# Optimization experiments

Hardware: AMD Instinct MI355X
Metric: run time of the kernel (lower is better)

The kernel has to match this reference:

```python
import jax, jax.numpy as jnp
import numpy as np

NEG = -1e9  # effective -inf in log space (finite to keep grads NaN-free)


def _forward_lattice(theta, A):
    """alpha[b,i,j,s]: log-prob of all alignments reaching cell (i,j) in state s.
    States: 0=match (diag move), 1=insert-x (down move), 2=insert-y (right move).
    alpha[i,j,s] = theta[i,j,s] + LSE_k(alpha[i-ds,j-dj,k] + A[k,s]).
    Start: only the match contribution at (0,0) gets log-prob 0."""
    B, N, M, S = theta.shape
    j_is0 = (jnp.arange(M) == 0)  # [M]

    def row_step(prev_row, xs):
        theta_row, i = xs  # theta_row: [B, M, S]
        # diag predecessor alpha[i-1, j-1, :]
        diag = jnp.concatenate(
            [jnp.full((B, 1, S), NEG, theta_row.dtype), prev_row[:, :-1]], axis=1)
        lse_m = jax.nn.logsumexp(diag + A[:, None, :, 0], axis=-1)      # [B, M]
        lse_m = jnp.where((i == 0) & j_is0[None, :], 0.0, lse_m)        # start at (0,0)
        lse_x = jax.nn.logsumexp(prev_row + A[:, None, :, 1], axis=-1)  # [B, M]
        m_vals = theta_row[:, :, 0] + lse_m
        x_vals = theta_row[:, :, 1] + lse_x
        th_y = theta_row[:, :, 2]

        def col_step(left, cxs):
            # left: alpha[i, j-1, :] -> [B, S]
            m_j, x_j, ty_j = cxs  # each [B]
            y_j = ty_j + jax.nn.logsumexp(left + A[:, :, 2], axis=-1)
            cell = jnp.stack([m_j, x_j, y_j], axis=-1)  # [B, S]
            return cell, cell

        left0 = jnp.full((B, S), NEG, theta_row.dtype)
        _, row = jax.lax.scan(col_step, left0, (m_vals.T, x_vals.T, th_y.T))
        row = jnp.transpose(row, (1, 0, 2))  # [B, M, S]
        return row, row

    prev0 = jnp.full((B, M, S), NEG, theta.dtype)
    _, alpha = jax.lax.scan(row_step, prev0, (jnp.swapaxes(theta, 0, 1), jnp.arange(N)))
    return jnp.swapaxes(alpha, 0, 1)  # [B, N, M, S]


def _backward_lattice(theta, A):
    """beta[b,i,j,s]: log-prob of all alignment suffixes from (i,j) in state s.
    beta[i,j,s] = LSE( A[s,0]+theta[i+1,j+1,0]+beta[i+1,j+1,0],
                       A[s,1]+theta[i+1,j,1]  +beta[i+1,j,1],
                       A[s,2]+theta[i,j+1,2]  +beta[i,j+1,2] ),  beta[N-1,M-1,:] = 0.
    Computed as a forward scan on the flipped grid with u = beta + theta."""
    B, N, M, S = theta.shape
    theta_f = theta[:, ::-1, ::-1]
    j_is0 = (jnp.arange(M) == 0)

    def row_step(u_prev, xs):
        th_row, p = xs  # th_row: [B, M, S] (flipped coords)
        t_m = jnp.concatenate(
            [jnp.full((B, 1), NEG, th_row.dtype), u_prev[:, :-1, 0]], axis=1)  # [B, M]
        t_x = u_prev[:, :, 1]  # [B, M]

        def col_step(left_u2, cxs):
            tm_j, tx_j, th_j, j0 = cxs  # [B], [B], [B,S], scalar bool
            v = jnp.stack([tm_j, tx_j, left_u2], axis=-1)     # [B, S] over successor k
            g = jax.nn.logsumexp(A + v[:, None, :], axis=-1)  # [B, S]
            g = jnp.where((p == 0) & j0, 0.0, g)              # terminal cell
            u = g + th_j
            return u[:, 2], (g, u)

        left0 = jnp.full((B,), NEG, th_row.dtype)
        _, (g_row, u_row) = jax.lax.scan(
            col_step, left0, (t_m.T, t_x.T, jnp.swapaxes(th_row, 0, 1), j_is0))
        return jnp.transpose(u_row, (1, 0, 2)), jnp.transpose(g_row, (1, 0, 2))

    u0 = jnp.full((B, M, S), NEG, theta.dtype)
    _, g = jax.lax.scan(row_step, u0, (jnp.swapaxes(theta_f, 0, 1), jnp.arange(N)))
    g = jnp.swapaxes(g, 0, 1)  # [B, N, M, S] flipped coords
    return g[:, ::-1, ::-1]


def setup_inputs() -> dict:
    key = jax.random.key(0)
    k1, k2 = jax.random.split(key)
    B, N, M, S = 256, 128, 128, 3
    theta = jax.random.normal(k1, (B, N, M, S), dtype=jnp.float32)
    A = jax.random.normal(k2, (B, S, S), dtype=jnp.float32)
    return {"theta": theta, "A": A}


def reference(theta, A):
    # Baum-Welch: posterior log-marginals gamma = alpha + beta - logZ
    alpha = _forward_lattice(theta, A)
    beta = _backward_lattice(theta, A)
    logZ = jax.nn.logsumexp(alpha[:, -1, -1, :], axis=-1)  # [B]
    return alpha + beta - logZ[:, None, None, None]
```

## Files before the change

kernel.cpp:

```cpp
#include <hip/hip_runtime.h>

#define HNEG (-1000000000.0f)
#define HNEG2 (-1.44269504e9f)
#define INVLN2 1.44269504088896341f
#define LN2F 0.69314718055994531f

constexpr int Nc = 128;
constexpr int Mc = 128;
constexpr int CELLS = Nc * Mc * 3;
constexpr int AWSTRIDE = CELLS + 16;

__device__ __forceinline__ float ex2(float x) {
  return __builtin_amdgcn_exp2f(x);
}
__device__ __forceinline__ float lg2(float x) {
  return __builtin_amdgcn_logf(x);
}

__device__ __forceinline__ float lse3(float a, float b, float c) {
  float mx = fmaxf(fmaxf(a, b), c);
  return mx + __logf(__expf(a - mx) + __expf(b - mx) + __expf(c - mx));
}

__device__ __forceinline__ float shr1f(float src, float fill) {
  return __int_as_float(__builtin_amdgcn_update_dpp(
      __float_as_int(fill), __float_as_int(src), 0x138, 0xF, 0xF, false));
}

__device__ __forceinline__ int clamp127(int i) {
  return i < 0 ? 0 : (i > 127 ? 127 : i);
}

__device__ __forceinline__ void st3_even(float* o, float a, float b, float c) {
  *(float2*)o = make_float2(a, b);
  o[2] = c;
}
__device__ __forceinline__ void st3_odd(float* o, float a, float b, float c) {
  o[0] = a;
  *(float2*)(o + 1) = make_float2(b, c);
}

#define DECL6(p) float p##0, p##1, p##2, p##3, p##4, p##5


#define F2LOAD(P, dd) do {                                                     \
    const int dc_ = (dd) > 254 ? 254 : (dd);                                   \
    const int ca_ = clamp127(dc_ - jA), cb_ = clamp127(dc_ - jB);              \
    const float* pa_ = th + (ca_ * Mc + jA) * 3;                               \
    const float* pb_ = th + (cb_ * Mc + jB) * 3;                               \
    P##0 = pa_[0]; P##1 = pa_[1]; P##2 = pa_[2];                               \
    P##3 = pb_[0]; P##4 = pb_[1]; P##5 = pb_[2];                               \
  } while (0)

#define F2STEP(P, dd) do {                                                     \
    const int iA_ = (dd) - jA, iB_ = (dd) - jB;                                \
    const bool okA_ = (unsigned)iA_ < (unsigned)Nc;                            \
    const bool okB_ = (unsigned)iB_ < (unsigned)Nc;                            \
    const float g0 = mS2 + lg2(wS20 * E00 + wS21 * E10 + wS22 * E20);          \
    const float g1 = mPA + lg2(wPA0 * E01 + wPA1 * E11 + wPA2 * E21);          \
    const float g2 = mS1 + lg2(wS10 * E02 + wS11 * E12 + wS12 * E22);          \
    const float cA0 = okA_ ? fmaf(P##0, INVLN2, g0) : HNEG2;                   \
    const float cA1 = okA_ ? fmaf(P##1, INVLN2, g1) : HNEG2;                   \
    const float cA2 = okA_ ? fmaf(P##2, INVLN2, g2) : HNEG2;                   \
    st3_even(okA_ ? aw + (iA_ * Mc + jA) * 3 : dmpE, cA0, cA1, cA2);           \
    const float h0 = mPP + lg2(wPP0 * E00 + wPP1 * E10 + wPP2 * E20);          \
    const float h1 = mPB + lg2(wPB0 * E01 + wPB1 * E11 + wPB2 * E21);          \
    const float h2 = mPA + lg2(wPA0 * E02 + wPA1 * E12 + wPA2 * E22);          \
    const float cB0 = okB_ ? fmaf(P##3, INVLN2, h0) : HNEG2;                   \
    const float cB1 = okB_ ? fmaf(P##4, INVLN2, h1) : HNEG2;                   \
    const float cB2 = okB_ ? fmaf(P##5, INVLN2, h2) : HNEG2;                   \
    st3_odd(okB_ ? aw + (iB_ * Mc + jB) * 3 : dmpO, cB0, cB1, cB2);            \
    const float mA_ = fmaxf(fmaxf(cA0, cA1), cA2);                             \
    const float a0_ = ex2(cA0 - mA_), a1_ = ex2(cA1 - mA_),                    \
                a2_ = ex2(cA2 - mA_);                                          \
    const float mB_ = fmaxf(fmaxf(cB0, cB1), cB2);                             \
    const float b0_ = ex2(cB0 - mB_), b1_ = ex2(cB1 - mB_),                    \
                b2_ = ex2(cB2 - mB_);                                          \
    mPP = mPA; wPP0 = wPA0; wPP1 = wPA1; wPP2 = wPA2;                          \
    mPA = mA_; wPA0 = a0_; wPA1 = a1_; wPA2 = a2_;                             \
    mPB = mB_; wPB0 = b0_; wPB1 = b1_; wPB2 = b2_;                             \
    mS2 = mS1; wS20 = wS10; wS21 = wS11; wS22 = wS12;                          \
    mS1 = shr1f(mB_, HNEG2);                                                   \
    wS10 = shr1f(b0_, 1.f); wS11 = shr1f(b1_, 1.f); wS12 = shr1f(b2_, 1.f);    \
  } while (0)

#define B2LOADL(Pt, dd) do {                                                   \
    int dor_ = 254 - (dd); if (dor_ < 0) dor_ = 0;                             \
    const int ca_ = clamp127(dor_ - jjA), cb_ = clamp127(dor_ - jjB);          \
    const float* pa_ = th + (ca_ * Mc + jjA) * 3;                              \
    const float* pb_ = th + (cb_ * Mc + jjB) * 3;                              \
    Pt##0 = pa_[0]; Pt##1 = pa_[1]; Pt##2 = pa_[2];                            \
    Pt##3 = pb_[0]; Pt##4 = pb_[1]; Pt##5 = pb_[2];                            \
  } while (0)

#define B2STEPL(Pt, dd) do {                                                   \
    const int iA_ = Nc - 1 - (dd) + jA;                                        \
    const int iB_ = Nc - 1 - (dd) + jB;                                        \
    const bool okA_ = (unsigned)iA_ < (unsigned)Nc;                            \
    const bool okB_ = (unsigned)iB_ < (unsigned)Nc;                            \
    float uA0, uA1, uA2, uB0, uB1, uB2;                                        \
    {                                                                          \
      const float v0 = S2u0, v1 = pAu1, v2 = S1u2;                             \
      const float mv = fmaxf(fmaxf(v0, v1), v2);                               \
      const float w0 = ex2(v0 - mv), w1 = ex2(v1 - mv), w2 = ex2(v2 - mv);     \
      float g0 = mv + lg2(w0 * E00 + w1 * E01 + w2 * E02);                     \
      float g1 = mv + lg2(w0 * E10 + w1 * E11 + w2 * E12);                     \
      float g2 = mv + lg2(w0 * E20 + w1 * E21 + w2 * E22);                     \
      if ((dd) == 0 && l == 0) { g0 = 0.f; g1 = 0.f; g2 = 0.f; }               \
      uA0 = okA_ ? fmaf(Pt##0, INVLN2, g0) : HNEG2;                            \
      uA1 = okA_ ? fmaf(Pt##1, INVLN2, g1) : HNEG2;                            \
      uA2 = okA_ ? fmaf(Pt##2, INVLN2, g2) : HNEG2;                            \
      st3_odd(okA_ ? ob + (iA_ * Mc + jjA) * 3 : dmpO, g0, g1, g2);            \
    }                                                                          \
    {                                                                          \
      const float v0 = ppAu0, v1 = pBu1, v2 = pAu2;                            \
      const float mv = fmaxf(fmaxf(v0, v1), v2);                               \
      const float w0 = ex2(v0 - mv), w1 = ex2(v1 - mv), w2 = ex2(v2 - mv);     \
      const float g0 = mv + lg2(w0 * E00 + w1 * E01 + w2 * E02);               \
      const float g1 = mv + lg2(w0 * E10 + w1 * E11 + w2 * E12);               \
      const float g2 = mv + lg2(w0 * E20 + w1 * E21 + w2 * E22);               \
      uB0 = okB_ ? fmaf(Pt##3, INVLN2, g0) : HNEG2;                            \
      uB1 = okB_ ? fmaf(Pt##4, INVLN2, g1) : HNEG2;                            \
      uB2 = okB_ ? fmaf(Pt##5, INVLN2, g2) : HNEG2;                            \
      st3_even(okB_ ? ob + (iB_ * Mc + jjB) * 3 : dmpE, g0, g1, g2);           \
    }                                                                          \
    ppAu0 = pAu0; pAu0 = uA0; pAu1 = uA1; pAu2 = uA2; pBu1 = uB1;              \
    S2u0 = S1u0;                                                               \
    S1u0 = shr1f(uB0, HNEG2);                                                  \
    S1u2 = shr1f(uB2, HNEG2);                                                  \
  } while (0)

__global__ __launch_bounds__(128, 1) void fbf_kernel(
    const float* __restrict__ theta, const float* __restrict__ A,
    float* __restrict__ aw_, float* __restrict__ ob_) {
  const int b = blockIdx.x;
  const int wave = threadIdx.x >> 6;
  const int l = threadIdx.x & 63;
  const float* th = theta + (size_t)b * CELLS;
  const float* Ab = A + b * 9;
  const float E00 = __expf(Ab[0]), E01 = __expf(Ab[1]), E02 = __expf(Ab[2]);
  const float E10 = __expf(Ab[3]), E11 = __expf(Ab[4]), E12 = __expf(Ab[5]);
  const float E20 = __expf(Ab[6]), E21 = __expf(Ab[7]), E22 = __expf(Ab[8]);

  __shared__ float sLZ;

  const int jA = 2 * l, jB = 2 * l + 1;
  float* aw = aw_ + (size_t)b * AWSTRIDE;
  float* ob = ob_ + (size_t)b * CELLS;
  float* dpad = aw + CELLS;

  if (wave == 0) {
    float* dmpE = dpad;
    float* dmpO = dpad + 3;

    float mPA = HNEG2, wPA0 = 1.f, wPA1 = 1.f, wPA2 = 1.f;
    float mPB = HNEG2, wPB0 = 1.f, wPB1 = 1.f, wPB2 = 1.f;
    float mPP = HNEG2, wPP0 = 1.f, wPP1 = 1.f, wPP2 = 1.f;
    float mS1 = HNEG2, wS10 = 1.f, wS11 = 1.f, wS12 = 1.f;
    float mS2 = HNEG2, wS20 = 1.f, wS21 = 1.f, wS22 = 1.f;
    if (l == 0) { mS2 = 0.f; wS20 = 1.0f / E00; wS21 = 0.f; wS22 = 0.f; }

    DECL6(xt0); DECL6(xt1); DECL6(xt2); DECL6(xt3);
    DECL6(yt0); DECL6(yt1); DECL6(yt2); DECL6(yt3);

    F2LOAD(xt0, 0); F2LOAD(xt1, 1); F2LOAD(xt2, 2); F2LOAD(xt3, 3);
    F2LOAD(yt0, 4); F2LOAD(yt1, 5); F2LOAD(yt2, 6); F2LOAD(yt3, 7);

    for (int t = 0; t < 31; ++t) {
      const int d0 = 8 * t;
      F2STEP(xt0, d0 + 0); F2STEP(xt1, d0 + 1); F2STEP(xt2, d0 + 2); F2STEP(xt3, d0 + 3);
      F2LOAD(xt0, d0 + 8); F2LOAD(xt1, d0 + 9); F2LOAD(xt2, d0 + 10); F2LOAD(xt3, d0 + 11);
      F2STEP(yt0, d0 + 4); F2STEP(yt1, d0 + 5); F2STEP(yt2, d0 + 6); F2STEP(yt3, d0 + 7);
      F2LOAD(yt0, d0 + 12); F2LOAD(yt1, d0 + 13); F2LOAD(yt2, d0 + 14); F2LOAD(yt3, d0 + 15);
    }
    F2STEP(xt0, 248); F2STEP(xt1, 249); F2STEP(xt2, 250); F2STEP(xt3, 251);
    F2STEP(yt0, 252); F2STEP(yt1, 253); F2STEP(yt2, 254);
    if (l == 63) sLZ = mPB + lg2(wPB0 + wPB1 + wPB2);
  } else {
    const int jjA = Mc - 1 - jA, jjB = Mc - 1 - jB;
    float* dmpE = dpad + 8;
    float* dmpO = dpad + 11;

    float pAu0 = HNEG2, pAu1 = HNEG2, pAu2 = HNEG2;
    float ppAu0 = HNEG2, pBu1 = HNEG2;
    float S1u0 = HNEG2, S1u2 = HNEG2, S2u0 = HNEG2;

    DECL6(xt0); DECL6(xt1); DECL6(xt2); DECL6(xt3);
    DECL6(yt0); DECL6(yt1); DECL6(yt2); DECL6(yt3);

    B2LOADL(xt0, 0); B2LOADL(xt1, 1); B2LOADL(xt2, 2); B2LOADL(xt3, 3);
    B2LOADL(yt0, 4); B2LOADL(yt1, 5); B2LOADL(yt2, 6); B2LOADL(yt3, 7);

    for (int t = 0; t < 31; ++t) {
      const int d0 = 8 * t;
      B2STEPL(xt0, d0 + 0); B2STEPL(xt1, d0 + 1);
      B2STEPL(xt2, d0 + 2); B2STEPL(xt3, d0 + 3);
      B2LOADL(xt0, d0 + 8); B2LOADL(xt1, d0 + 9);
      B2LOADL(xt2, d0 + 10); B2LOADL(xt3, d0 + 11);
      B2STEPL(yt0, d0 + 4); B2STEPL(yt1, d0 + 5);
      B2STEPL(yt2, d0 + 6); B2STEPL(yt3, d0 + 7);
      B2LOADL(yt0, d0 + 12); B2LOADL(yt1, d0 + 13);
      B2LOADL(yt2, d0 + 14); B2LOADL(yt3, d0 + 15);
    }
    B2STEPL(xt0, 248); B2STEPL(xt1, 249); B2STEPL(xt2, 250); B2STEPL(xt3, 251);
    B2STEPL(yt0, 252); B2STEPL(yt1, 253); B2STEPL(yt2, 254);
  }

  __syncthreads();
  const float lz = sLZ;
  const float4* a4 = (const float4*)aw;
  float4* o4 = (float4*)ob;
#pragma unroll 4
  for (int k = threadIdx.x; k < CELLS / 4; k += 128) {
    const float4 a = a4[k];
    const float4 g = o4[k];
    o4[k] = make_float4((a.x + g.x - lz) * LN2F, (a.y + g.y - lz) * LN2F,
                        (a.z + g.z - lz) * LN2F, (a.w + g.w - lz) * LN2F);
  }
}

__global__ __launch_bounds__(128) void fwd_fb(const float* __restrict__ theta,
                                              const float* __restrict__ A,
                                              float* __restrict__ out) {
  const int b = blockIdx.x;
  const int j = threadIdx.x;
  const float* th = theta + (size_t)b * CELLS;
  float* ob = out + (size_t)b * CELLS;

  __shared__ float sA[9];
  __shared__ float ring[3][Mc + 1][3];
  if (j < 9) sA[j] = A[b * 9 + j];
  {
    float* rf = &ring[0][0][0];
    for (int t = j; t < 3 * (Mc + 1) * 3; t += Mc) rf[t] = HNEG;
  }
  __syncthreads();
  const float A00 = sA[0], A01 = sA[1], A02 = sA[2];
  const float A10 = sA[3], A11 = sA[4], A12 = sA[5];
  const float A20 = sA[6], A21 = sA[7], A22 = sA[8];

  float p0 = HNEG, p1 = HNEG, p2 = HNEG;
  float tc0 = 0.f, tc1 = 0.f, tc2 = 0.f, tn0 = 0.f, tn1 = 0.f, tn2 = 0.f;
  if (j == 0) { tc0 = th[0]; tc1 = th[1]; tc2 = th[2]; }
  if (j <= 1) {
    const int i1 = 1 - j;
    const float* p = th + (i1 * Mc + j) * 3;
    tn0 = p[0]; tn1 = p[1]; tn2 = p[2];
  }
  int s0 = 0, s1 = 2, s2 = 1;
  for (int d = 0; d < Nc + Mc - 1; ++d) {
    const int i = d - j;
    float tf0 = 0.f, tf1 = 0.f, tf2 = 0.f;
    const int ip = i + 2;
    if (ip >= 0 && ip < Nc) {
      const float* p = th + (ip * Mc + j) * 3;
      tf0 = p[0]; tf1 = p[1]; tf2 = p[2];
    }
    float c0 = HNEG, c1 = HNEG, c2 = HNEG;
    if (i >= 0 && i < Nc) {
      const float* nd1 = ring[s1][j];
      const float* nd2 = ring[s2][j];
      float lm = lse3(nd2[0] + A00, nd2[1] + A10, nd2[2] + A20);
      if (i == 0 && j == 0) lm = 0.0f;
      float lx = lse3(p0 + A01, p1 + A11, p2 + A21);
      float ly = lse3(nd1[0] + A02, nd1[1] + A12, nd1[2] + A22);
      c0 = tc0 + lm; c1 = tc1 + lx; c2 = tc2 + ly;
      float* o = ob + (i * Mc + j) * 3;
      o[0] = c0; o[1] = c1; o[2] = c2;
    }
    float* w = ring[s0][j + 1];
    w[0] = c0; w[1] = c1; w[2] = c2;
    __syncthreads();
    p0 = c0; p1 = c1; p2 = c2;
    tc0 = tn0; tc1 = tn1; tc2 = tn2;
    tn0 = tf0; tn1 = tf1; tn2 = tf2;
    const int t = s2; s2 = s1; s1 = s0; s0 = t;
  }
}

__global__ __launch_bounds__(128) void bwd_fb(const float* __restrict__ theta,
                                              const float* __restrict__ A,
                                              float* __restrict__ ob_) {
  const int b = blockIdx.x;
  const int q = threadIdx.x;
  const float* th = theta + (size_t)b * CELLS;
  float* ob = ob_ + (size_t)b * CELLS;

  __shared__ float sA[9];
  __shared__ float ring[3][Mc + 1][3];
  __shared__ float sZ;
  if (q < 9) sA[q] = A[b * 9 + q];
  {
    float* rf = &ring[0][0][0];
    for (int t = q; t < 3 * (Mc + 1) * 3; t += Mc) rf[t] = HNEG;
  }
  if (q == 0) {
    sZ = lse3(ob[(Nc * Mc - 1) * 3 + 0], ob[(Nc * Mc - 1) * 3 + 1],
              ob[(Nc * Mc - 1) * 3 + 2]);
  }
  __syncthreads();
  const float A00 = sA[0], A01 = sA[1], A02 = sA[2];
  const float A10 = sA[3], A11 = sA[4], A12 = sA[5];
  const float A20 = sA[6], A21 = sA[7], A22 = sA[8];
  const float logZ = sZ;

  const int jj = Mc - 1 - q;
  float pu1 = HNEG;
  float tc0 = 0.f, tc1 = 0.f, tc2 = 0.f, tn0 = 0.f, tn1 = 0.f, tn2 = 0.f;
  float ac0 = 0.f, ac1 = 0.f, ac2 = 0.f, an0 = 0.f, an1 = 0.f, an2 = 0.f;
  if (q == 0) {
    const float* p = th + ((Nc - 1) * Mc + jj) * 3;
    tc0 = p[0]; tc1 = p[1]; tc2 = p[2];
    const float* a = ob + ((Nc - 1) * Mc + jj) * 3;
    ac0 = a[0]; ac1 = a[1]; ac2 = a[2];
  }
  if (q <= 1) {
    const int i1 = Nc - 2 + q;
    const float* p = th + (i1 * Mc + jj) * 3;
    tn0 = p[0]; tn1 = p[1]; tn2 = p[2];
    const float* a = ob + (i1 * Mc + jj) * 3;
    an0 = a[0]; an1 = a[1]; an2 = a[2];
  }
  int s0 = 0, s1 = 2, s2 = 1;
  for (int d = 0; d < Nc + Mc - 1; ++d) {
    const int p = d - q;
    const int i = Nc - 1 - p;
    float tf0 = 0.f, tf1 = 0.f, tf2 = 0.f, af0 = 0.f, af1 = 0.f, af2 = 0.f;
    const int ipf = i - 2;
    if (ipf >= 0 && ipf < Nc) {
      const float* pp = th + (ipf * Mc + jj) * 3;
      tf0 = pp[0]; tf1 = pp[1]; tf2 = pp[2];
      const float* aa = ob + (ipf * Mc + jj) * 3;
      af0 = aa[0]; af1 = aa[1]; af2 = aa[2];
    }
    float u0 = HNEG, u1 = HNEG, u2 = HNEG;
    if (p >= 0 && p < Nc) {
      const float* nd1 = ring[s1][q];
      const float* nd2 = ring[s2][q];
      const float v0 = nd2[0];
      const float v1 = pu1;
      const float v2 = nd1[2];
      float g0 = lse3(A00 + v0, A01 + v1, A02 + v2);
      float g1 = lse3(A10 + v0, A11 + v1, A12 + v2);
      float g2 = lse3(A20 + v0, A21 + v1, A22 + v2);
      if (p == 0 && q == 0) { g0 = 0.0f; g1 = 0.0f; g2 = 0.0f; }
      u0 = g0 + tc0; u1 = g1 + tc1; u2 = g2 + tc2;
      float* o = ob + (i * Mc + jj) * 3;
      o[0] = ac0 + g0 - logZ;
      o[1] = ac1 + g1 - logZ;
      o[2] = ac2 + g2 - logZ;
    }
    float* w = ring[s0][q + 1];
    w[0] = u0; w[1] = u1; w[2] = u2;
    __syncthreads();
    pu1 = u1;
    tc0 = tn0; tc1 = tn1; tc2 = tn2;
    tn0 = tf0; tn1 = tf1; tn2 = tf2;
    ac0 = an0; ac1 = an1; ac2 = an2;
    an0 = af0; an1 = af1; an2 = af2;
    const int t = s2; s2 = s1; s1 = s0; s0 = t;
  }
}

extern "C" void kernel_launch(void* const* d_in, const int* in_sizes, int n_in,
                              void* d_out, int out_size, void* d_ws, size_t ws_size,
                              hipStream_t stream) {
  const float* theta = (const float*)d_in[0];
  const float* A = (const float*)d_in[1];
  float* out = (float*)d_out;
  const int B = in_sizes[1] / 9;

  const size_t need = (size_t)B * AWSTRIDE * 4;
  if (ws_size >= need) {
    float* aw = (float*)d_ws;
    fbf_kernel<<<dim3(B), dim3(128), 0, stream>>>(theta, A, aw, out);
  } else {
    fwd_fb<<<dim3(B), dim3(128), 0, stream>>>(theta, A, out);
    bwd_fb<<<dim3(B), dim3(128), 0, stream>>>(theta, A, out);
  }
}
```

Before: 203.4 us.

## Split final alpha+beta combine into a separate wide-grid kernel

The fused kernel no longer runs the final elementwise combine with only 128 threads per batch after the DP. Instead it writes logZ to workspace, and a second kernel with a grid of B x 12 blocks of 256 threads does the combine. The aim is to spread this bandwidth-bound pass across many more waves and CUs instead of two waves per block. The cost is an extra kernel launch and one more pass of reads through global memory between kernels.

Result: slower. 211.9 us (+4.2%).

```diff
diff --git a/kernel.cpp b/kernel.cpp
--- a/kernel.cpp
+++ b/kernel.cpp
@@ -130,9 +130,10 @@
     S1u2 = shr1f(uB2, HNEG2);                                                  \
   } while (0)
 
-__global__ __launch_bounds__(128, 1) void fbf_kernel(
+__global__ __launch_bounds__(128, 1) void fb_dp_kernel(
     const float* __restrict__ theta, const float* __restrict__ A,
-    float* __restrict__ aw_, float* __restrict__ ob_) {
+    float* __restrict__ aw_, float* __restrict__ logZ_ws,
+    float* __restrict__ ob_) {
   const int b = blockIdx.x;
   const int wave = threadIdx.x >> 6;
   const int l = threadIdx.x & 63;
@@ -142,8 +143,6 @@
   const float E10 = __expf(Ab[3]), E11 = __expf(Ab[4]), E12 = __expf(Ab[5]);
   const float E20 = __expf(Ab[6]), E21 = __expf(Ab[7]), E22 = __expf(Ab[8]);
 
-  __shared__ float sLZ;
-
   const int jA = 2 * l, jB = 2 * l + 1;
   float* aw = aw_ + (size_t)b * AWSTRIDE;
   float* ob = ob_ + (size_t)b * CELLS;
@@ -175,7 +174,7 @@
     }
     F2STEP(xt0, 248); F2STEP(xt1, 249); F2STEP(xt2, 250); F2STEP(xt3, 251);
     F2STEP(yt0, 252); F2STEP(yt1, 253); F2STEP(yt2, 254);
-    if (l == 63) sLZ = mPB + lg2(wPB0 + wPB1 + wPB2);
+    if (l == 63) logZ_ws[b] = mPB + lg2(wPB0 + wPB1 + wPB2);
   } else {
     const int jjA = Mc - 1 - jA, jjB = Mc - 1 - jB;
     float* dmpE = dpad + 8;
@@ -205,17 +204,24 @@
     B2STEPL(xt0, 248); B2STEPL(xt1, 249); B2STEPL(xt2, 250); B2STEPL(xt3, 251);
     B2STEPL(yt0, 252); B2STEPL(yt1, 253); B2STEPL(yt2, 254);
   }
-
-  __syncthreads();
-  const float lz = sLZ;
-  const float4* a4 = (const float4*)aw;
-  float4* o4 = (float4*)ob;
-#pragma unroll 4
-  for (int k = threadIdx.x; k < CELLS / 4; k += 128) {
-    const float4 a = a4[k];
-    const float4 g = o4[k];
-    o4[k] = make_float4((a.x + g.x - lz) * LN2F, (a.y + g.y - lz) * LN2F,
-                        (a.z + g.z - lz) * LN2F, (a.w + g.w - lz) * LN2F);
+}
+
+__global__ __launch_bounds__(256) void combine_kernel(
+    const float4* __restrict__ aw4, const float* __restrict__ logZ_ws,
+    float4* __restrict__ out4) {
+  const int b = blockIdx.x;
+  const float lz = logZ_ws[b];
+  const int off = blockIdx.y * 1024 + threadIdx.x;
+  const size_t ab = (size_t)b * (AWSTRIDE / 4);
+  const size_t obx = (size_t)b * 12288;
+#pragma unroll
+  for (int k = 0; k < 4; ++k) {
+    const size_t i = off + (size_t)k * 256;
+    const float4 a = aw4[ab + i];
+    const float4 g = out4[obx + i];
+    out4[obx + i] =
+        make_float4((a.x + g.x - lz) * LN2F, (a.y + g.y - lz) * LN2F,
+                    (a.z + g.z - lz) * LN2F, (a.w + g.w - lz) * LN2F);
   }
 }
 
@@ -370,10 +376,13 @@
   float* out = (float*)d_out;
   const int B = in_sizes[1] / 9;
 
-  const size_t need = (size_t)B * AWSTRIDE * 4;
+  const size_t need = (size_t)B * (AWSTRIDE + 1) * 4;
   if (ws_size >= need) {
     float* aw = (float*)d_ws;
-    fbf_kernel<<<dim3(B), dim3(128), 0, stream>>>(theta, A, aw, out);
+    float* logZ_ws = aw + (size_t)B * AWSTRIDE;
+    fb_dp_kernel<<<dim3(B), dim3(128), 0, stream>>>(theta, A, aw, logZ_ws, out);
+    combine_kernel<<<dim3(B, 12), dim3(256), 0, stream>>>(
+        (const float4*)aw, logZ_ws, (float4*)out);
   } else {
     fwd_fb<<<dim3(B), dim3(128), 0, stream>>>(theta, A, out);
     bwd_fb<<<dim3(B), dim3(128), 0, stream>>>(theta, A, out);
```
